# Performance work log

Measured on AMD Instinct MI355X. Metric: run time of the kernel, lower is better.

The kernel has to match this reference:

```python
import jax, jax.numpy as jnp
import numpy as np

B, N, E, D = 8, 2048, 4096, 256
HOPS = 3

def setup_inputs() -> dict:
    key = jax.random.key(0)
    ks = jax.random.split(key, 12)
    p = lambda k, shp: (jax.random.normal(k, shp, dtype=jnp.float32) * 0.02)
    return {
        "node_vec": jax.random.normal(ks[0], (B, N, D), dtype=jnp.float32),
        "edge_vec": jax.random.normal(ks[1], (B, E, D), dtype=jnp.float32),
        "node2edge": jax.random.uniform(ks[2], (B, E, N), dtype=jnp.float32),
        "edge2node": jax.random.uniform(ks[3], (B, N, E), dtype=jnp.float32),
        "node_mask": jnp.ones((B, N), dtype=jnp.float32),
        "W_fuse": p(ks[4], (D, 2 * D)), "b_fuse": jnp.zeros((D,), jnp.float32),
        "W_z": p(ks[5], (D, 4 * D)), "b_z": jnp.zeros((D,), jnp.float32),
        "W_update": p(ks[6], (D, 2 * D)),
        "W_reset": p(ks[7], (D, 2 * D)),
        "W_memory": p(ks[8], (D, 2 * D)),
        "W_max": p(ks[9], (D, D)),
    }

def _gnn_step(node_vec, edge_vec, n2e, e2n, W_fuse, b_fuse):
    # n2e: [B,E,N], e2n: [B,N,E]
    edge_emb = jnp.einsum('ben,bnd->bed', n2e, node_vec)          # [B,E,D]
    edge_emb = jax.nn.relu(jnp.concatenate([edge_emb, edge_vec], axis=-1) @ W_fuse.T + b_fuse)
    norm = jnp.sum(e2n, axis=2, keepdims=True) + 1.0               # [B,N,1]
    return (jnp.einsum('bne,bed->bnd', e2n, edge_emb) + node_vec) / norm

def _gated_fusion(in_vec, out_vec, W_z, b_z):
    feats = jnp.concatenate([in_vec, out_vec, in_vec * out_vec, in_vec - out_vec], axis=-1)
    z = jax.nn.sigmoid(feats @ W_z.T + b_z)
    return (1.0 - z) * in_vec + z * out_vec

def _gru_step(cur, new, W_u, W_r, W_m):
    cn = jnp.concatenate([cur, new], axis=-1)
    u = jax.nn.sigmoid(cn @ W_u.T)
    r = jax.nn.sigmoid(cn @ W_r.T)
    m = jnp.tanh(jnp.concatenate([r * cur, new], axis=-1) @ W_m.T)
    return (1.0 - u) * cur + u * m

def reference(node_vec, edge_vec, node2edge, edge2node, node_mask,
              W_fuse, b_fuse, W_z, b_z, W_update, W_reset, W_memory, W_max):
    n2e_T = jnp.swapaxes(node2edge, 1, 2)  # [B,N,E]
    e2n_T = jnp.swapaxes(edge2node, 1, 2)  # [B,E,N]
    for _ in range(HOPS):
        out_vec = _gnn_step(node_vec, edge_vec, node2edge, edge2node, W_fuse, b_fuse)
        in_vec = _gnn_step(node_vec, edge_vec, e2n_T, n2e_T, W_fuse, b_fuse)
        new_vec = _gated_fusion(in_vec, out_vec, W_z, b_z)
        node_vec = _gru_step(node_vec, new_vec, W_update, W_reset, W_memory)
    # graph max-pooling: linear then max over nodes (node_mask unused, as in original)
    graph_embedding = jnp.max(node_vec @ W_max.T, axis=1)          # [B,D]
    return (jnp.swapaxes(node_vec, 0, 1), graph_embedding[None])    # [N,B,D], [1,B,D]
```

## Files before the change

kernel.cpp:

```cpp
#include <hip/hip_runtime.h>
#include <math.h>

#define Bb 8
#define Nn 2048
#define Ee 4096
#define Dd 256
#define HOPS 3

typedef __attribute__((ext_vector_type(4))) float f32x4;
typedef _Float16 f16;
typedef __attribute__((ext_vector_type(8))) _Float16 f16x8;
typedef __attribute__((ext_vector_type(4))) _Float16 f16x4;
typedef __attribute__((ext_vector_type(8))) short s16x8;
typedef __attribute__((ext_vector_type(4))) short s16x4;

__device__ __forceinline__ short f2bf(float f){
  union{float f; unsigned u;} x; x.f=f;
  unsigned r = (x.u + 0x7fffu + ((x.u>>16)&1u)) >> 16;
  return (short)r;
}
__device__ __forceinline__ float bf2f(short h){
  union{unsigned u; float f;} x; x.u = ((unsigned)(unsigned short)h) << 16; return x.f;
}
__device__ __forceinline__ int swz(int row, int idx){ return idx ^ ((row & 7) << 3); }

enum { HN=0, HT=1 };
enum { OF=0, OH=1, OHT=2 };
enum { EP_NONE=0, EP_BIAS, EP_ADDRELU, EP_AGG };
enum { SM_CN=0, SM_G4, SM_RC };
enum { SE_GATE=0, SE_SIG, SE_TANH };

template<int AMODE, bool AH, int SPL, int EPI, int OUTM>
__global__ __launch_bounds__(512) void hgemm(
    const void* __restrict__ Av, const f16* __restrict__ Bh, void* __restrict__ Cv,
    const float* __restrict__ aux1, const float* __restrict__ aux2,
    const float* __restrict__ bias,
    int M, int Nd, int K, int lda, int ldb, int ldc,
    long sA, long sB, long sC, long sAux1, long sAux2,
    long aLo, long bLo, int maskB, int mask1)
{
  const int bz = blockIdx.z;
  const char* Ab = (const char*)Av + (AH ? bz * sA * 2 : bz * sA * 4);
  Bh += (long)(bz & maskB) * sB;
  char* Cb = (char*)Cv + ((OUTM == OF) ? bz * sC * 4 : bz * sC * 2);
  if (aux1) aux1 += (long)(bz & mask1) * sAux1;
  if (aux2) aux2 += bz * sAux2;
  const int m0 = blockIdx.y * 128;
  const int n0 = blockIdx.x * 128;

  constexpr int HLA = 128 * 64;
  constexpr int HLB = 128 * 64;
  __shared__ f16 As[128 * 64 * ((SPL & 2) ? 2 : 1)];
  __shared__ f16 Bs[128 * 64 * ((SPL & 1) ? 2 : 1)];

  const int tid = threadIdx.x;
  const int wid = tid >> 6, lane = tid & 63;
  const int wm = (wid >> 1) * 32, wn = (wid & 1) * 64;
  const int r = lane & 15, g = lane >> 4;

  f32x4 acc[2][4];
  #pragma unroll
  for (int i = 0; i < 2; i++)
    #pragma unroll
    for (int j = 0; j < 4; j++) acc[i][j] = (f32x4){0.f, 0.f, 0.f, 0.f};

  f16x8 ra0, ra1, rl0, rl1;
  f16x8 rb0, rb1, rbl0, rbl1;

  auto loadA = [&](int k0) {
    if (AMODE == HN && AH) {
      const f16* Ah = (const f16*)Ab;
      const int row = tid >> 2, kc = (tid & 3) * 16;
      const long off = (long)(m0 + row) * lda + k0 + kc;
      ra0 = *(const f16x8*)&Ah[off];
      ra1 = *(const f16x8*)&Ah[off + 8];
      if (SPL & 2) { rl0 = *(const f16x8*)&Ah[aLo + off]; rl1 = *(const f16x8*)&Ah[aLo + off + 8]; }
    } else if (AMODE == HN && !AH) {
      const float* Af = (const float*)Ab;
      const int row = tid >> 2, kc = (tid & 3) * 16;
      const float* s = &Af[(long)(m0 + row) * lda + k0 + kc];
      f32x4 v0 = *(const f32x4*)s,       v1 = *(const f32x4*)(s + 4);
      f32x4 v2 = *(const f32x4*)(s + 8), v3 = *(const f32x4*)(s + 12);
      ra0 = (f16x8){(f16)v0.x,(f16)v0.y,(f16)v0.z,(f16)v0.w,(f16)v1.x,(f16)v1.y,(f16)v1.z,(f16)v1.w};
      ra1 = (f16x8){(f16)v2.x,(f16)v2.y,(f16)v2.z,(f16)v2.w,(f16)v3.x,(f16)v3.y,(f16)v3.z,(f16)v3.w};
    } else {
      const int mm = tid & 127, kh = (tid >> 7) * 16;
      if (AH) {
        const f16* s = &((const f16*)Ab)[(long)(k0 + kh) * lda + m0 + mm];
        #pragma unroll
        for (int j = 0; j < 8; j++) ra0[j] = s[(long)j * lda];
        #pragma unroll
        for (int j = 0; j < 8; j++) ra1[j] = s[(long)(j + 8) * lda];
      } else {
        const float* s = &((const float*)Ab)[(long)(k0 + kh) * lda + m0 + mm];
        #pragma unroll
        for (int j = 0; j < 8; j++) ra0[j] = (f16)s[(long)j * lda];
        #pragma unroll
        for (int j = 0; j < 8; j++) ra1[j] = (f16)s[(long)(j + 8) * lda];
      }
    }
  };
  auto storeA = [&]() {
    if (AMODE == HT) {
      const int mm = tid & 127, kh = (tid >> 7) * 16;
      *(f16x8*)&As[swz(mm, mm * 64 + kh)]     = ra0;
      *(f16x8*)&As[swz(mm, mm * 64 + kh + 8)] = ra1;
    } else {
      const int row = tid >> 2, kc = (tid & 3) * 16;
      const int i0 = swz(row, row * 64 + kc), i1 = swz(row, row * 64 + kc + 8);
      *(f16x8*)&As[i0] = ra0;
      *(f16x8*)&As[i1] = ra1;
      if (SPL & 2) { *(f16x8*)&As[HLA + i0] = rl0; *(f16x8*)&As[HLA + i1] = rl1; }
    }
  };
  auto loadB = [&](int k0) {
    const int row = tid >> 2, kc = (tid & 3) * 16;
    const long off = (long)(n0 + row) * ldb + k0 + kc;
    rb0 = *(const f16x8*)&Bh[off];
    rb1 = *(const f16x8*)&Bh[off + 8];
    if (SPL & 1) { rbl0 = *(const f16x8*)&Bh[bLo + off]; rbl1 = *(const f16x8*)&Bh[bLo + off + 8]; }
  };
  auto storeB = [&]() {
    const int row = tid >> 2, kc = (tid & 3) * 16;
    const int i0 = swz(row, row * 64 + kc), i1 = swz(row, row * 64 + kc + 8);
    *(f16x8*)&Bs[i0] = rb0;
    *(f16x8*)&Bs[i1] = rb1;
    if (SPL & 1) { *(f16x8*)&Bs[HLB + i0] = rbl0; *(f16x8*)&Bs[HLB + i1] = rbl1; }
  };

  loadA(0); loadB(0);
  storeA(); storeB();
  __syncthreads();

  const int NT = K >> 6;
  for (int t = 0; t < NT; t++) {
    const bool more = (t + 1 < NT);
    if (more) { loadA((t + 1) << 6); loadB((t + 1) << 6); }
    #pragma unroll
    for (int ks = 0; ks < 2; ks++) {
      f16x8 af[2], bf[4], afl[2], bfl[4];
      #pragma unroll
      for (int i = 0; i < 2; i++) {
        const int rw = wm + i * 16 + r;
        const int ix = swz(rw, rw * 64 + ks * 32 + g * 8);
        af[i] = *(const f16x8*)&As[ix];
        if (SPL & 2) afl[i] = *(const f16x8*)&As[HLA + ix];
      }
      #pragma unroll
      for (int j = 0; j < 4; j++) {
        const int rw = wn + j * 16 + r;
        const int ix = swz(rw, rw * 64 + ks * 32 + g * 8);
        bf[j] = *(const f16x8*)&Bs[ix];
        if (SPL & 1) bfl[j] = *(const f16x8*)&Bs[HLB + ix];
      }
      #pragma unroll
      for (int i = 0; i < 2; i++)
        #pragma unroll
        for (int j = 0; j < 4; j++) {
          acc[i][j] = __builtin_amdgcn_mfma_f32_16x16x32_f16(af[i], bf[j], acc[i][j], 0, 0, 0);
          if (SPL & 1)
            acc[i][j] = __builtin_amdgcn_mfma_f32_16x16x32_f16(af[i], bfl[j], acc[i][j], 0, 0, 0);
          if (SPL & 2)
            acc[i][j] = __builtin_amdgcn_mfma_f32_16x16x32_f16(afl[i], bf[j], acc[i][j], 0, 0, 0);
        }
    }
    __syncthreads();
    if (more) { storeA(); storeB(); __syncthreads(); }
  }

  if (OUTM == OHT) {
    f16* tile = (f16*)Bs;
    #pragma unroll
    for (int half = 0; half < 2; half++) {
      __syncthreads();
      if ((wm >> 6) == half) {
        #pragma unroll
        for (int i = 0; i < 2; i++)
          #pragma unroll
          for (int j = 0; j < 4; j++) {
            const int rowl = wm + i * 16 + g * 4 - 64 * half;
            const int coll = wn + j * 16 + r;
            #pragma unroll
            for (int t = 0; t < 4; t++) {
              float v = acc[i][j][t];
              if (EPI == EP_ADDRELU) {
                v += aux1[(long)(m0 + 64 * half + rowl + t) * 256 + n0 + coll];
                v = v > 0.f ? v : 0.f;
              } else if (EPI == EP_BIAS) { v += bias[n0 + coll]; }
              tile[coll * 72 + rowl + t] = (f16)v;
            }
          }
      }
      __syncthreads();
      const int c2 = tid >> 2, rs = (tid & 3) * 16;
      f16* dst = &((f16*)Cb)[(long)(n0 + c2) * ldc + m0 + 64 * half + rs];
      *(f16x8*)dst       = *(const f16x8*)&tile[c2 * 72 + rs];
      *(f16x8*)(dst + 8) = *(const f16x8*)&tile[c2 * 72 + rs + 8];
    }
  } else {
    #pragma unroll
    for (int i = 0; i < 2; i++) {
      #pragma unroll
      for (int j = 0; j < 4; j++) {
        const int rowb = m0 + wm + i * 16 + g * 4;
        const int col = n0 + wn + j * 16 + r;
        #pragma unroll
        for (int t = 0; t < 4; t++) {
          const int row = rowb + t;
          const long idx = (long)row * ldc + col;
          float v = acc[i][j][t];
          if (EPI == EP_BIAS)         { v += bias[col]; }
          else if (EPI == EP_ADDRELU) { v += aux1[(long)row * 256 + col]; v = v > 0.f ? v : 0.f; }
          else if (EPI == EP_AGG)     { v = (v + aux1[idx]) * aux2[row]; }
          if (OUTM == OH) ((f16*)Cb)[idx] = (f16)v;
          else            ((float*)Cb)[idx] = v;
        }
      }
    }
  }
}

template<int AMODE, int EPI>
__global__ __launch_bounds__(256) void ggemm(
    const float* __restrict__ A, const float* __restrict__ A2, const float* __restrict__ A3,
    const short* __restrict__ Bw, float* __restrict__ C,
    const float* __restrict__ aux1, const float* __restrict__ aux2, const float* __restrict__ bias,
    int Nd, int K, int lda, int ldb, int ldc, long bLo)
{
  const int m0 = blockIdx.y * 64;
  const int n0 = blockIdx.x * 128;
  constexpr int HLA = 64 * 64;
  constexpr int HLB = 128 * 64;
  __shared__ short As[64 * 64 * 2];
  __shared__ short Bs[128 * 64 * 2];

  const int tid = threadIdx.x;
  const int wid = tid >> 6, lane = tid & 63;
  const int wm = (wid >> 1) * 32, wn = (wid & 1) * 64;
  const int r = lane & 15, g = lane >> 4;

  f32x4 acc[2][4];
  #pragma unroll
  for (int i = 0; i < 2; i++)
    #pragma unroll
    for (int j = 0; j < 4; j++) acc[i][j] = (f32x4){0.f, 0.f, 0.f, 0.f};

  s16x4 rah[4], ral[4];
  s16x8 rbh[4], rbl[4];

  auto loadA = [&](int k0) {
    const int row = tid >> 2, kc = (tid & 3) * 16;
    const int kk = k0 + kc, q = kk >> 8, kd = kk & 255;
    const long base = (long)(m0 + row) * 256 + kd;
    const long baseA = (long)(m0 + row) * lda + kd;
    #pragma unroll
    for (int u = 0; u < 4; u++) {
      f32x4 v;
      if (AMODE == SM_CN) {
        v = (q == 0) ? *(const f32x4*)(A + base + 4 * u)
                     : *(const f32x4*)(A2 + base + 4 * u);
      } else if (AMODE == SM_G4) {
        if (q == 0)      v = *(const f32x4*)(A  + base + 4 * u);
        else if (q == 1) v = *(const f32x4*)(A2 + base + 4 * u);
        else {
          f32x4 x = *(const f32x4*)(A  + base + 4 * u);
          f32x4 y = *(const f32x4*)(A2 + base + 4 * u);
          v = (q == 2) ? x * y : x - y;
        }
      } else {
        if (q == 0) {
          f32x4 x = *(const f32x4*)(A  + baseA + 4 * u);
          f32x4 y = *(const f32x4*)(A2 + base + 4 * u);
          v = x * y;
        } else v = *(const f32x4*)(A3 + base + 4 * u);
      }
      s16x4 h = { f2bf(v.x), f2bf(v.y), f2bf(v.z), f2bf(v.w) };
      rah[u] = h;
      ral[u] = (s16x4){ f2bf(v.x - bf2f(h.x)), f2bf(v.y - bf2f(h.y)),
                        f2bf(v.z - bf2f(h.z)), f2bf(v.w - bf2f(h.w)) };
    }
  };
  auto storeA = [&]() {
    const int row = tid >> 2, kc = (tid & 3) * 16;
    const int i0 = swz(row, row * 64 + kc), i1 = swz(row, row * 64 + kc + 8);
    *(s16x4*)&As[i0]     = rah[0]; *(s16x4*)&As[i0 + 4] = rah[1];
    *(s16x4*)&As[i1]     = rah[2]; *(s16x4*)&As[i1 + 4] = rah[3];
    *(s16x4*)&As[HLA + i0]     = ral[0]; *(s16x4*)&As[HLA + i0 + 4] = ral[1];
    *(s16x4*)&As[HLA + i1]     = ral[2]; *(s16x4*)&As[HLA + i1 + 4] = ral[3];
  };
  auto loadB = [&](int k0) {
    const int row = tid >> 1, kc = (tid & 1) * 32;
    const long off = (long)(n0 + row) * ldb + k0 + kc;
    #pragma unroll
    for (int u = 0; u < 4; u++) {
      rbh[u] = *(const s16x8*)&Bw[off + 8 * u];
      rbl[u] = *(const s16x8*)&Bw[bLo + off + 8 * u];
    }
  };
  auto storeB = [&]() {
    const int row = tid >> 1, kc = (tid & 1) * 32;
    #pragma unroll
    for (int u = 0; u < 4; u++) {
      const int bx = swz(row, row * 64 + kc + 8 * u);
      *(s16x8*)&Bs[bx] = rbh[u];
      *(s16x8*)&Bs[HLB + bx] = rbl[u];
    }
  };

  loadA(0); loadB(0);
  storeA(); storeB();
  __syncthreads();

  const int NT = K >> 6;
  for (int t = 0; t < NT; t++) {
    const bool more = (t + 1 < NT);
    if (more) { loadA((t + 1) << 6); loadB((t + 1) << 6); }
    #pragma unroll
    for (int ks = 0; ks < 2; ks++) {
      s16x8 ah[2], al[2], bh[4], bl[4];
      #pragma unroll
      for (int i = 0; i < 2; i++) {
        const int rw = wm + i * 16 + r;
        const int ix = swz(rw, rw * 64 + ks * 32 + g * 8);
        ah[i] = *(const s16x8*)&As[ix];
        al[i] = *(const s16x8*)&As[HLA + ix];
      }
      #pragma unroll
      for (int j = 0; j < 4; j++) {
        const int rw = wn + j * 16 + r;
        const int ix = swz(rw, rw * 64 + ks * 32 + g * 8);
        bh[j] = *(const s16x8*)&Bs[ix];
        bl[j] = *(const s16x8*)&Bs[HLB + ix];
      }
      #pragma unroll
      for (int i = 0; i < 2; i++)
        #pragma unroll
        for (int j = 0; j < 4; j++) {
          acc[i][j] = __builtin_amdgcn_mfma_f32_16x16x32_bf16(ah[i], bh[j], acc[i][j], 0, 0, 0);
          acc[i][j] = __builtin_amdgcn_mfma_f32_16x16x32_bf16(ah[i], bl[j], acc[i][j], 0, 0, 0);
          acc[i][j] = __builtin_amdgcn_mfma_f32_16x16x32_bf16(al[i], bh[j], acc[i][j], 0, 0, 0);
        }
    }
    __syncthreads();
    if (more) { storeA(); storeB(); __syncthreads(); }
  }

  #pragma unroll
  for (int i = 0; i < 2; i++) {
    #pragma unroll
    for (int j = 0; j < 4; j++) {
      #pragma unroll
      for (int t = 0; t < 4; t++) {
        const int row = m0 + wm + i * 16 + g * 4 + t;
        const int col = n0 + wn + j * 16 + r;
        float v = acc[i][j][t];
        if (EPI == SE_GATE) {
          v += bias[col];
          float z = 1.f / (1.f + __expf(-v));
          const long ix = (long)row * 256 + col;
          v = (1.f - z) * aux1[ix] + z * aux2[ix];
        } else if (EPI == SE_SIG) {
          v = 1.f / (1.f + __expf(-v));
        } else {
          v = tanhf(v);
        }
        C[(long)row * ldc + col] = v;
      }
    }
  }
}


__global__ void cvt_n2e_colsum(const float* __restrict__ n2e, f16* __restrict__ n2e_h,
                               float* __restrict__ part) {
  const int n = blockIdx.x * 256 + threadIdx.x;
  const int c = blockIdx.y, b = blockIdx.z;
  const long base = (long)b * Ee * Nn + (long)c * 256 * Nn + n;
  float s = 0.f;
  for (int e = 0; e < 256; e++) {
    float v = n2e[base + (long)e * Nn];
    n2e_h[base + (long)e * Nn] = (f16)v;
    s += v;
  }
  part[((long)b * 16 + c) * Nn + n] = s;
}

__global__ void cvt_e2n_rowsum(const float* __restrict__ e2n, f16* __restrict__ e2n_h,
                               float* __restrict__ rno) {
  const long row = blockIdx.x;
  const int tid = threadIdx.x, lane = tid & 63, wid = tid >> 6;
  const float* p = e2n + row * Ee;
  f16* ph = e2n_h + row * Ee;
  float s = 0.f;
  for (int e = tid; e < Ee; e += 256) { float v = p[e]; ph[e] = (f16)v; s += v; }
  #pragma unroll
  for (int off = 32; off; off >>= 1) s += __shfl_down(s, off);
  __shared__ float wsum[4];
  if (lane == 0) wsum[wid] = s;
  __syncthreads();
  if (tid == 0) rno[row] = 1.f / (1.f + wsum[0] + wsum[1] + wsum[2] + wsum[3]);
}

__global__ void adjT(const f16* __restrict__ in, f16* __restrict__ out, int R, int C) {
  __shared__ f16 t[64][72];
  const long boff = (long)blockIdx.z * R * C;
  const int r0 = blockIdx.x * 64, c0 = blockIdx.y * 64;
  const int tid = threadIdx.x;
  const int rl = tid >> 2, cl = (tid & 3) * 16;
  const f16* src = in + boff + (long)(r0 + rl) * C + c0 + cl;
  *(f16x8*)&t[rl][cl]     = *(const f16x8*)src;
  *(f16x8*)&t[rl][cl + 8] = *(const f16x8*)(src + 8);
  __syncthreads();
  const int cl2 = tid >> 2, rl2 = (tid & 3) * 16;
  f16x8 o0, o1;
  #pragma unroll
  for (int v = 0; v < 8; v++) { o0[v] = t[rl2 + v][cl2]; o1[v] = t[rl2 + 8 + v][cl2]; }
  f16* dst = out + boff + (long)(c0 + cl2) * R + r0 + rl2;
  *(f16x8*)dst = o0;
  *(f16x8*)(dst + 8) = o1;
}

__global__ void rowsum_kernel(const float* __restrict__ e2n, float* __restrict__ out) {
  const int gw = blockIdx.x * 4 + (threadIdx.x >> 6);
  const int lane = threadIdx.x & 63;
  const float* p = e2n + (long)gw * Ee;
  float s = 0.f;
  for (int e = lane; e < Ee; e += 64) s += p[e];
  #pragma unroll
  for (int off = 32; off; off >>= 1) s += __shfl_down(s, off);
  if (lane == 0) out[gw] = 1.f / (1.f + s);
}
__global__ void colsum_kernel(const float* __restrict__ n2e, float* __restrict__ part) {
  const int n = blockIdx.x * 256 + threadIdx.x;
  const int c = blockIdx.y, b = blockIdx.z;
  const float* p = n2e + (long)b * Ee * Nn + (long)c * 256 * Nn + n;
  float s = 0.f;
  for (int e = 0; e < 256; e++) s += p[(long)e * Nn];
  part[((long)b * 16 + c) * Nn + n] = s;
}
__global__ void colfin_kernel(const float* __restrict__ part, float* __restrict__ rni) {
  const int i = blockIdx.x * 256 + threadIdx.x;
  const int b = i >> 11, n = i & 2047;
  float s = 0.f;
  #pragma unroll
  for (int c = 0; c < 16; c++) s += part[((long)b * 16 + c) * Nn + n];
  rni[i] = 1.f / (1.f + s);
}

__global__ void cvt_half(const float* __restrict__ src, f16* __restrict__ dst) {
  const long i4 = (long)blockIdx.x * 256 + threadIdx.x;
  f32x4 v = *(const f32x4*)&src[i4 * 4];
  *(f16x4*)&dst[i4 * 4] = (f16x4){(f16)v.x, (f16)v.y, (f16)v.z, (f16)v.w};
}

__global__ void cvt_half_split(const float* __restrict__ src, f16* __restrict__ dst, long loOff) {
  const long i4 = (long)blockIdx.x * 256 + threadIdx.x;
  f32x4 v = *(const f32x4*)&src[i4 * 4];
  f16x4 h = {(f16)v.x, (f16)v.y, (f16)v.z, (f16)v.w};
  *(f16x4*)&dst[i4 * 4] = h;
  f16x4 l = {(f16)(v.x - (float)h[0]), (f16)(v.y - (float)h[1]),
             (f16)(v.z - (float)h[2]), (f16)(v.w - (float)h[3])};
  *(f16x4*)&dst[loOff + i4 * 4] = l;
}

__global__ void cvt_bf_split(const float* __restrict__ src, short* __restrict__ dst, long loOff) {
  const long i4 = (long)blockIdx.x * 256 + threadIdx.x;
  f32x4 v = *(const f32x4*)&src[i4 * 4];
  s16x4 h = { f2bf(v.x), f2bf(v.y), f2bf(v.z), f2bf(v.w) };
  *(s16x4*)&dst[i4 * 4] = h;
  s16x4 l = { f2bf(v.x - bf2f(h.x)), f2bf(v.y - bf2f(h.y)),
              f2bf(v.z - bf2f(h.z)), f2bf(v.w - bf2f(h.w)) };
  *(s16x4*)&dst[loOff + i4 * 4] = l;
}

__global__ void init_cur(const float* __restrict__ node_vec, float* __restrict__ cur,
                         f16* __restrict__ cur_h, long loOff) {
  const long i4 = (long)blockIdx.x * 256 + threadIdx.x;
  f32x4 v = *(const f32x4*)&node_vec[i4 * 4];
  *(f32x4*)&cur[i4 * 4] = v;
  f16x4 h = {(f16)v.x, (f16)v.y, (f16)v.z, (f16)v.w};
  *(f16x4*)&cur_h[i4 * 4] = h;
  f16x4 l = {(f16)(v.x - (float)h[0]), (f16)(v.y - (float)h[1]),
             (f16)(v.z - (float)h[2]), (f16)(v.w - (float)h[3])};
  *(f16x4*)&cur_h[loOff + i4 * 4] = l;
}

__global__ void transposeT(const float* __restrict__ cur, f16* __restrict__ curT, long loOff) {
  __shared__ f16 th[64][72];
  __shared__ f16 tl[64][72];
  const int b = blockIdx.z, nt = blockIdx.x * 64, dt = blockIdx.y * 64;
  const int tid = threadIdx.x;
  const int nl = tid >> 2, d0 = (tid & 3) * 16;
  const float* src = cur + ((long)b * Nn + nt + nl) * 256 + dt + d0;
  #pragma unroll
  for (int u = 0; u < 4; u++) {
    f32x4 v = *(const f32x4*)(src + 4 * u);
    f16x4 h = {(f16)v.x, (f16)v.y, (f16)v.z, (f16)v.w};
    *(f16x4*)&th[nl][d0 + 4 * u] = h;
    f16x4 l = {(f16)(v.x - (float)h[0]), (f16)(v.y - (float)h[1]),
               (f16)(v.z - (float)h[2]), (f16)(v.w - (float)h[3])};
    *(f16x4*)&tl[nl][d0 + 4 * u] = l;
  }
  __syncthreads();
  const int dl = tid >> 2, n0l = (tid & 3) * 16;
  f16x8 o0, o1, p0, p1;
  #pragma unroll
  for (int v = 0; v < 8; v++) {
    o0[v] = th[n0l + v][dl];     o1[v] = th[n0l + 8 + v][dl];
    p0[v] = tl[n0l + v][dl];     p1[v] = tl[n0l + 8 + v][dl];
  }
  f16* dst = curT + (long)b * (256 * Nn) + (long)(dt + dl) * Nn + nt + n0l;
  *(f16x8*)dst = o0;
  *(f16x8*)(dst + 8) = o1;
  *(f16x8*)(dst + loOff) = p0;
  *(f16x8*)(dst + loOff + 8) = p1;
}

__global__ void gruf_kernel(const float* __restrict__ urb, const float* __restrict__ m,
                            float* __restrict__ cur, f16* __restrict__ cur_h, long loOff) {
  const long i = (long)blockIdx.x * 256 + threadIdx.x;
  const long bn = i >> 8; const int d = i & 255;
  const float uu = urb[bn * 512 + d];
  const float v = (1.f - uu) * cur[i] + uu * m[i];
  cur[i] = v;
  f16 h = (f16)v;
  cur_h[i] = h;
  cur_h[loOff + i] = (f16)(v - (float)h);
}

__global__ void maxpool1(const float* __restrict__ pooled, float* __restrict__ part) {
  const int d = threadIdx.x, c = blockIdx.x, b = blockIdx.y;
  const float* p = pooled + ((long)b * Nn + c * 256) * Dd + d;
  float m = -INFINITY;
  for (int n = 0; n < 256; n++) m = fmaxf(m, p[(long)n * Dd]);
  part[(b * 8 + c) * Dd + d] = m;
}
__global__ void maxpool2(const float* __restrict__ part, float* __restrict__ out1) {
  const int d = threadIdx.x, b = blockIdx.x;
  float m = -INFINITY;
  #pragma unroll
  for (int c = 0; c < 8; c++) m = fmaxf(m, part[(b * 8 + c) * Dd + d]);
  out1[b * Dd + d] = m;
}
__global__ void transpose_out(const float* __restrict__ cur, float* __restrict__ out0) {
  const long i = (long)blockIdx.x * 256 + threadIdx.x;
  const int d = i & 255;
  const long nb = i >> 8;
  const int b = nb & 7;
  const long n = nb >> 3;
  out0[i] = cur[((long)b * Nn + n) * Dd + d];
}

extern "C" void kernel_launch(void* const* d_in, const int* in_sizes, int n_in,
                              void* d_out, int out_size, void* d_ws, size_t ws_size,
                              hipStream_t stream) {
  const float* node_vec = (const float*)d_in[0];
  const float* edge_vec = (const float*)d_in[1];
  const float* n2e      = (const float*)d_in[2];
  const float* e2n      = (const float*)d_in[3];
  const float* W_fuse   = (const float*)d_in[5];
  const float* b_fuse   = (const float*)d_in[6];
  const float* W_z      = (const float*)d_in[7];
  const float* b_z      = (const float*)d_in[8];
  const float* W_u      = (const float*)d_in[9];
  const float* W_r      = (const float*)d_in[10];
  const float* W_m      = (const float*)d_in[11];
  const float* W_max    = (const float*)d_in[12];

  const long ND  = (long)Bb * Nn * Dd;
  const long EDb = (long)Ee * Dd;
  const long NDb = (long)Nn * Dd;
  const long ED  = (long)Bb * EDb;
  const long ADJb = (long)Ee * Nn;
  const long ADJ = (long)Bb * ADJb;
  const int  BN  = Bb * Nn;

  char* p = (char*)d_ws;
  auto alloc = [&](size_t bytes) { char* r = p; p += (bytes + 255) & ~(size_t)255; return r; };

  const size_t need_full =
      (size_t)4 * ADJ * 2
      + (size_t)ED * 2
      + (size_t)4 * ED * 2
      + (size_t)ED * 4
      + (size_t)4 * ND * 2
      + (size_t)(2 * 131072 + 2 * 65536) * 2
      + (size_t)(2 * 262144 + 2 * 262144 + 2 * 131072) * 2
      + (size_t)5 * ND * 4
      + (size_t)BN * 512 * 4
      + (size_t)(2 * BN + 16 * BN + BN) * 4
      + 64 * 1024;
  const bool full = ws_size >= need_full;

  f16 *adjEO = nullptr, *adjAG = nullptr;
  f16 *n2e_h = nullptr, *e2n_hT = nullptr, *e2n_h = nullptr, *n2e_hT = nullptr;
  if (full) {
    adjEO = (f16*)alloc((size_t)2 * ADJ * 2);
    adjAG = (f16*)alloc((size_t)2 * ADJ * 2);
    n2e_h = adjEO;  e2n_hT = adjEO + ADJ;
    e2n_h = adjAG;  n2e_hT = adjAG + ADJ;
  }
  f16* ev_h    = (f16*)alloc(ED * 2);
  f16* E1h2    = (f16*)alloc((size_t)2 * ED * 2);
  f16* E2T2    = (f16*)alloc((size_t)2 * ED * 2);
  float* EVW   = (float*)alloc(ED * 4);
  f16* cur_h   = (f16*)alloc(2 * ND * 2);
  f16* cur_hT  = (f16*)alloc(2 * ND * 2);
  f16* Wf_h    = (f16*)alloc(2 * 131072 * 2);
  f16* Wmax_h  = (f16*)alloc(2 * 65536 * 2);
  short* Wz_s  = (short*)alloc((size_t)2 * 262144 * 2);
  short* Wur_s = (short*)alloc((size_t)2 * 262144 * 2);
  short* Wm_s  = (short*)alloc((size_t)2 * 131072 * 2);
  float* cur   = (float*)alloc(ND * 4);
  float* outv  = (float*)alloc(2 * ND * 4);
  float* inv   = outv + ND;
  float* nv    = (float*)alloc(ND * 4);
  float* urb   = (float*)alloc((size_t)BN * 512 * 4);
  float* mb    = (float*)alloc(ND * 4);
  float* rno   = (float*)alloc(2 * BN * 4);
  float* rni   = rno + BN;
  float* colpart = (float*)alloc((size_t)16 * BN * 4);
  float* maxpart = (float*)alloc(BN * 4);

  float* out0 = (float*)d_out;
  float* out1 = out0 + ND;

  if (full) {
    cvt_n2e_colsum<<<dim3(Nn / 256, 16, Bb), 256, 0, stream>>>(n2e, n2e_h, colpart);
    colfin_kernel<<<BN / 256, 256, 0, stream>>>(colpart, rni);
    cvt_e2n_rowsum<<<BN, 256, 0, stream>>>(e2n, e2n_h, rno);
    adjT<<<dim3(Ee / 64, Nn / 64, Bb), 256, 0, stream>>>(n2e_h, n2e_hT, Ee, Nn);
    adjT<<<dim3(Nn / 64, Ee / 64, Bb), 256, 0, stream>>>(e2n_h, e2n_hT, Nn, Ee);
  } else {
    colsum_kernel<<<dim3(Nn / 256, 16, Bb), 256, 0, stream>>>(n2e, colpart);
    colfin_kernel<<<BN / 256, 256, 0, stream>>>(colpart, rni);
    rowsum_kernel<<<BN / 4, 256, 0, stream>>>(e2n, rno);
  }
  cvt_half<<<(int)(ED / 1024), 256, 0, stream>>>(edge_vec, ev_h);
  cvt_half_split<<<131072 / 1024, 256, 0, stream>>>(W_fuse, Wf_h, 131072);
  cvt_half_split<<<65536 / 1024, 256, 0, stream>>>(W_max, Wmax_h, 65536);
  cvt_bf_split<<<262144 / 1024, 256, 0, stream>>>(W_z, Wz_s, 262144);
  cvt_bf_split<<<131072 / 1024, 256, 0, stream>>>(W_u, Wur_s, 262144);
  cvt_bf_split<<<131072 / 1024, 256, 0, stream>>>(W_r, Wur_s + 131072, 262144);
  cvt_bf_split<<<131072 / 1024, 256, 0, stream>>>(W_m, Wm_s, 131072);
  init_cur<<<(int)(ND / 1024), 256, 0, stream>>>(node_vec, cur, cur_h, ND);
  transposeT<<<dim3(Nn / 64, 4, Bb), 256, 0, stream>>>(cur, cur_hT, ND);

  hgemm<HN, true, 1, EP_BIAS, OF><<<dim3(2, Ee / 128, Bb), 512, 0, stream>>>(
      ev_h, Wf_h + 256, EVW, nullptr, nullptr, b_fuse,
      Ee, 256, 256, 256, 512, 256, EDb, 0, EDb, 0, 0, 0, 131072, 0, 0);

  for (int h = 0; h < HOPS; h++) {
    if (full) {
      hgemm<HN, true, 1, EP_NONE, OH><<<dim3(2, Ee / 128, 2 * Bb), 512, 0, stream>>>(
          adjEO, cur_hT, E1h2, nullptr, nullptr, nullptr,
          Ee, 256, Nn, Nn, Nn, 256, ADJb, NDb, EDb, 0, 0, 0, ND, 7, 0);
      hgemm<HN, true, 1, EP_ADDRELU, OHT><<<dim3(2, Ee / 128, 2 * Bb), 512, 0, stream>>>(
          E1h2, Wf_h, E2T2, EVW, nullptr, nullptr,
          Ee, 256, 256, 256, 512, Ee, EDb, 0, EDb, EDb, 0, 0, 131072, 0, 7);
      hgemm<HN, true, 0, EP_AGG, OF><<<dim3(2, Nn / 128, 2 * Bb), 512, 0, stream>>>(
          adjAG, E2T2, outv, cur, rno, nullptr,
          Nn, 256, Ee, Ee, Ee, 256, ADJb, EDb, NDb, NDb, (long)Nn, 0, 0, 15, 7);
    } else {
      hgemm<HN, false, 1, EP_NONE, OH><<<dim3(2, Ee / 128, Bb), 512, 0, stream>>>(
          n2e, cur_hT, E1h2, nullptr, nullptr, nullptr,
          Ee, 256, Nn, Nn, Nn, 256, ADJb, NDb, EDb, 0, 0, 0, ND, 7, 0);
      hgemm<HT, false, 1, EP_NONE, OH><<<dim3(2, Ee / 128, Bb), 512, 0, stream>>>(
          e2n, cur_hT, E1h2 + ED, nullptr, nullptr, nullptr,
          Ee, 256, Nn, Ee, Nn, 256, ADJb, NDb, EDb, 0, 0, 0, ND, 7, 0);
      hgemm<HN, true, 1, EP_ADDRELU, OHT><<<dim3(2, Ee / 128, 2 * Bb), 512, 0, stream>>>(
          E1h2, Wf_h, E2T2, EVW, nullptr, nullptr,
          Ee, 256, 256, 256, 512, Ee, EDb, 0, EDb, EDb, 0, 0, 131072, 0, 7);
      hgemm<HN, false, 0, EP_AGG, OF><<<dim3(2, Nn / 128, Bb), 512, 0, stream>>>(
          e2n, E2T2, outv, cur, rno, nullptr,
          Nn, 256, Ee, Ee, Ee, 256, (long)Nn * Ee, EDb, NDb, NDb, (long)Nn, 0, 0, 15, 7);
      hgemm<HT, false, 0, EP_AGG, OF><<<dim3(2, Nn / 128, Bb), 512, 0, stream>>>(
          n2e, E2T2 + ED, inv, cur, rni, nullptr,
          Nn, 256, Ee, Nn, Ee, 256, (long)Ee * Nn, EDb, NDb, NDb, (long)Nn, 0, 0, 15, 7);
    }
    ggemm<SM_G4, SE_GATE><<<dim3(2, BN / 64, 1), 256, 0, stream>>>(
        inv, outv, nullptr, Wz_s, nv, inv, outv, b_z, 256, 1024, 256, 1024, 256, 262144);
    ggemm<SM_CN, SE_SIG><<<dim3(4, BN / 64, 1), 256, 0, stream>>>(
        cur, nv, nullptr, Wur_s, urb, nullptr, nullptr, nullptr, 512, 512, 256, 512, 512, 262144);
    ggemm<SM_RC, SE_TANH><<<dim3(2, BN / 64, 1), 256, 0, stream>>>(
        urb + 256, cur, nv, Wm_s, mb, nullptr, nullptr, nullptr, 256, 512, 512, 512, 256, 131072);
    gruf_kernel<<<(int)(ND / 256), 256, 0, stream>>>(urb, mb, cur, cur_h, ND);
    if (h < HOPS - 1)
      transposeT<<<dim3(Nn / 64, 4, Bb), 256, 0, stream>>>(cur, cur_hT, ND);
  }

  hgemm<HN, true, 3, EP_NONE, OF><<<dim3(2, BN / 128, 1), 512, 0, stream>>>(
      cur_h, Wmax_h, urb, nullptr, nullptr, nullptr,
      BN, 256, 256, 256, 256, 256, 0, 0, 0, 0, 0, ND, 65536, 0, 0);
  maxpool1<<<dim3(8, Bb), 256, 0, stream>>>(urb, maxpart);
  maxpool2<<<Bb, 256, 0, stream>>>(maxpart, out1);

  transpose_out<<<(int)(ND / 256), 256, 0, stream>>>(cur, out0);
}
```

Measured before the change: 1.688 ms.

## Double-buffer global prefetch registers two tiles ahead and raise MFMA priority

The GEMM main loop now keeps two register sets for global loads, so tile t+2 is being fetched while tile t is computed and tile t+1 waits in registers. This lets global memory latency hide behind two compute stages instead of one. The MFMA section is also wrapped in s_setprio(1)/s_setprio(0) so the scheduler favours matrix work. The extra register sets raise VGPR pressure and may lower occupancy.

```diff
diff --git a/kernel.cpp b/kernel.cpp
--- a/kernel.cpp
+++ b/kernel.cpp
@@ -64,78 +64,71 @@
     #pragma unroll
     for (int j = 0; j < 4; j++) acc[i][j] = (f32x4){0.f, 0.f, 0.f, 0.f};
 
-  f16x8 ra0, ra1, rl0, rl1;
-  f16x8 rb0, rb1, rbl0, rbl1;
-
-  auto loadA = [&](int k0) {
+  f16x8 aA0, aA1, aL0, aL1, bA0, bA1, bL0, bL1;
+  f16x8 aB0, aB1, aM0, aM1, bB0, bB1, bM0, bM1;
+
+  auto loadA = [&](int k0, f16x8& o0, f16x8& o1, f16x8& l0, f16x8& l1) {
     if (AMODE == HN && AH) {
       const f16* Ah = (const f16*)Ab;
       const int row = tid >> 2, kc = (tid & 3) * 16;
       const long off = (long)(m0 + row) * lda + k0 + kc;
-      ra0 = *(const f16x8*)&Ah[off];
-      ra1 = *(const f16x8*)&Ah[off + 8];
-      if (SPL & 2) { rl0 = *(const f16x8*)&Ah[aLo + off]; rl1 = *(const f16x8*)&Ah[aLo + off + 8]; }
+      o0 = *(const f16x8*)&Ah[off];
+      o1 = *(const f16x8*)&Ah[off + 8];
+      if (SPL & 2) { l0 = *(const f16x8*)&Ah[aLo + off]; l1 = *(const f16x8*)&Ah[aLo + off + 8]; }
     } else if (AMODE == HN && !AH) {
       const float* Af = (const float*)Ab;
       const int row = tid >> 2, kc = (tid & 3) * 16;
       const float* s = &Af[(long)(m0 + row) * lda + k0 + kc];
       f32x4 v0 = *(const f32x4*)s,       v1 = *(const f32x4*)(s + 4);
       f32x4 v2 = *(const f32x4*)(s + 8), v3 = *(const f32x4*)(s + 12);
-      ra0 = (f16x8){(f16)v0.x,(f16)v0.y,(f16)v0.z,(f16)v0.w,(f16)v1.x,(f16)v1.y,(f16)v1.z,(f16)v1.w};
-      ra1 = (f16x8){(f16)v2.x,(f16)v2.y,(f16)v2.z,(f16)v2.w,(f16)v3.x,(f16)v3.y,(f16)v3.z,(f16)v3.w};
+      o0 = (f16x8){(f16)v0.x,(f16)v0.y,(f16)v0.z,(f16)v0.w,(f16)v1.x,(f16)v1.y,(f16)v1.z,(f16)v1.w};
+      o1 = (f16x8){(f16)v2.x,(f16)v2.y,(f16)v2.z,(f16)v2.w,(f16)v3.x,(f16)v3.y,(f16)v3.z,(f16)v3.w};
     } else {
       const int mm = tid & 127, kh = (tid >> 7) * 16;
       if (AH) {
         const f16* s = &((const f16*)Ab)[(long)(k0 + kh) * lda + m0 + mm];
         #pragma unroll
-        for (int j = 0; j < 8; j++) ra0[j] = s[(long)j * lda];
+        for (int j = 0; j < 8; j++) o0[j] = s[(long)j * lda];
         #pragma unroll
-        for (int j = 0; j < 8; j++) ra1[j] = s[(long)(j + 8) * lda];
+        for (int j = 0; j < 8; j++) o1[j] = s[(long)(j + 8) * lda];
       } else {
         const float* s = &((const float*)Ab)[(long)(k0 + kh) * lda + m0 + mm];
         #pragma unroll
-        for (int j = 0; j < 8; j++) ra0[j] = (f16)s[(long)j * lda];
+        for (int j = 0; j < 8; j++) o0[j] = (f16)s[(long)j * lda];
         #pragma unroll
-        for (int j = 0; j < 8; j++) ra1[j] = (f16)s[(long)(j + 8) * lda];
-      }
-    }
-  };
-  auto storeA = [&]() {
+        for (int j = 0; j < 8; j++) o1[j] = (f16)s[(long)(j + 8) * lda];
+      }
+    }
+  };
+  auto storeA = [&](f16x8& o0, f16x8& o1, f16x8& l0, f16x8& l1) {
     if (AMODE == HT) {
       const int mm = tid & 127, kh = (tid >> 7) * 16;
-      *(f16x8*)&As[swz(mm, mm * 64 + kh)]     = ra0;
-      *(f16x8*)&As[swz(mm, mm * 64 + kh + 8)] = ra1;
+      *(f16x8*)&As[swz(mm, mm * 64 + kh)]     = o0;
+      *(f16x8*)&As[swz(mm, mm * 64 + kh + 8)] = o1;
     } else {
       const int row = tid >> 2, kc = (tid & 3) * 16;
       const int i0 = swz(row, row * 64 + kc), i1 = swz(row, row * 64 + kc + 8);
-      *(f16x8*)&As[i0] = ra0;
-      *(f16x8*)&As[i1] = ra1;
-      if (SPL & 2) { *(f16x8*)&As[HLA + i0] = rl0; *(f16x8*)&As[HLA + i1] = rl1; }
-    }
-  };
-  auto loadB = [&](int k0) {
+      *(f16x8*)&As[i0] = o0;
+      *(f16x8*)&As[i1] = o1;
+      if (SPL & 2) { *(f16x8*)&As[HLA + i0] = l0; *(f16x8*)&As[HLA + i1] = l1; }
+    }
+  };
+  auto loadB = [&](int k0, f16x8& o0, f16x8& o1, f16x8& l0, f16x8& l1) {
     const int row = tid >> 2, kc = (tid & 3) * 16;
     const long off = (long)(n0 + row) * ldb + k0 + kc;
-    rb0 = *(const f16x8*)&Bh[off];
-    rb1 = *(const f16x8*)&Bh[off + 8];
-    if (SPL & 1) { rbl0 = *(const f16x8*)&Bh[bLo + off]; rbl1 = *(const f16x8*)&Bh[bLo + off + 8]; }
-  };
-  auto storeB = [&]() {
+    o0 = *(const f16x8*)&Bh[off];
+    o1 = *(const f16x8*)&Bh[off + 8];
+    if (SPL & 1) { l0 = *(const f16x8*)&Bh[bLo + off]; l1 = *(const f16x8*)&Bh[bLo + off + 8]; }
+  };
+  auto storeB = [&](f16x8& o0, f16x8& o1, f16x8& l0, f16x8& l1) {
     const int row = tid >> 2, kc = (tid & 3) * 16;
     const int i0 = swz(row, row * 64 + kc), i1 = swz(row, row * 64 + kc + 8);
-    *(f16x8*)&Bs[i0] = rb0;
-    *(f16x8*)&Bs[i1] = rb1;
-    if (SPL & 1) { *(f16x8*)&Bs[HLB + i0] = rbl0; *(f16x8*)&Bs[HLB + i1] = rbl1; }
-  };
-
-  loadA(0); loadB(0);
-  storeA(); storeB();
-  __syncthreads();
-
-  const int NT = K >> 6;
-  for (int t = 0; t < NT; t++) {
-    const bool more = (t + 1 < NT);
-    if (more) { loadA((t + 1) << 6); loadB((t + 1) << 6); }
+    *(f16x8*)&Bs[i0] = o0;
+    *(f16x8*)&Bs[i1] = o1;
+    if (SPL & 1) { *(f16x8*)&Bs[HLB + i0] = l0; *(f16x8*)&Bs[HLB + i1] = l1; }
+  };
+  auto mfmaTile = [&]() {
+    __builtin_amdgcn_s_setprio(1);
     #pragma unroll
     for (int ks = 0; ks < 2; ks++) {
       f16x8 af[2], bf[4], afl[2], bfl[4];
@@ -164,8 +157,27 @@
             acc[i][j] = __builtin_amdgcn_mfma_f32_16x16x32_f16(afl[i], bf[j], acc[i][j], 0, 0, 0);
         }
     }
+    __builtin_amdgcn_s_setprio(0);
+  };
+
+  const int NT = K >> 6;
+  loadA(0, aA0, aA1, aL0, aL1); loadB(0, bA0, bA1, bL0, bL1);
+  storeA(aA0, aA1, aL0, aL1);   storeB(bA0, bA1, bL0, bL1);
+  __syncthreads();
+  if (NT > 1) { loadA(64, aB0, aB1, aM0, aM1); loadB(64, bB0, bB1, bM0, bM1); }
+
+  for (int t = 0; t < NT; t += 2) {
+    if (t + 2 < NT) { loadA((t + 2) << 6, aA0, aA1, aL0, aL1); loadB((t + 2) << 6, bA0, bA1, bL0, bL1); }
+    mfmaTile();
     __syncthreads();
-    if (more) { storeA(); storeB(); __syncthreads(); }
+    if (t + 1 < NT) {
+      storeA(aB0, aB1, aM0, aM1); storeB(bB0, bB1, bM0, bM1);
+      __syncthreads();
+      if (t + 3 < NT) { loadA((t + 3) << 6, aB0, aB1, aM0, aM1); loadB((t + 3) << 6, bB0, bB1, bM0, bM1); }
+      mfmaTile();
+      __syncthreads();
+      if (t + 2 < NT) { storeA(aA0, aA1, aL0, aL1); storeB(bA0, bA1, bL0, bL1); __syncthreads(); }
+    }
   }
 
   if (OUTM == OHT) {
```

After: 1.791 ms. +6.1%, slower.
